# Kernel optimization log

Measured on AMD Instinct MI355X. Metric: run time of the kernel, lower is better.

Reference implementation:

```python
import jax, jax.numpy as jnp
import numpy as np

N_HEAD = 12
TOP_M = 16
MIN_SIZE = 2
MAX_SIZE = 8
ALPHA = 1.0
EPS = 1e-6

# Note: in the torch source, minimize_det=True and minimize_det=False select the
# identical subset (the sign flip in the score is exactly undone by flipping the
# comparisons), so we implement the single equivalent rule: maximize
# s = -log(det(K_S K_S^T) + 1e-6) / |S|**alpha.

def _token(qi, i, k_all, v_all):
    """Greedy DPP subset selection for one query token i. qi:[d], k_all/v_all:[T,d]."""
    T, d = k_all.shape
    slots = jnp.arange(MAX_SIZE)
    sim = k_all @ qi
    sim = jnp.where(jnp.arange(T) <= i, sim, -jnp.inf)  # causal mask
    vals, topidx = jax.lax.top_k(sim, TOP_M)
    avail0 = jnp.isfinite(vals) & (topidx != i)  # i is removed from candidates
    k_cand = k_all[topidx]                        # [M,d]
    cand_norm = jnp.sum(k_cand * k_cand, axis=-1)  # [M]
    ki = k_all[i]
    sel0 = jnp.zeros((MAX_SIZE,), jnp.int32).at[0].set(i.astype(jnp.int32))
    s0 = jax.lax.stop_gradient(-jnp.log(jnp.dot(ki, ki) + EPS))  # |S|=1 => size^alpha=1

    def body(state, _):
        sel, count, cur_s, avail, done = state
        # E: selected key vectors in slots < count, zeros elsewhere
        E = jnp.where((slots < count)[:, None], k_all[sel], 0.0)  # [S,d]
        G0 = E @ E.T                                              # [S,S]
        cross = k_cand @ E.T  # [M,S]; column `count` is 0 since that E row is 0
        u = (slots == count).astype(E.dtype)  # one-hot insertion slot
        # Gram of S u {c} for every candidate c, identity-padded beyond slot count
        grams = (G0[None]
                 + u[None, :, None] * cross[:, None, :]
                 + cross[:, :, None] * u[None, None, :]
                 + cand_norm[:, None, None] * (u[:, None] * u[None, :])[None])
        grams = grams + jnp.diag(jnp.where(slots > count, 1.0, 0.0))[None]
        det = jnp.linalg.det(grams.astype(jnp.float32))  # [M]
        s = -jnp.log(det + EPS) / (count + 1).astype(jnp.float32) ** ALPHA
        s = jax.lax.stop_gradient(jnp.where(avail, s, -jnp.inf))
        best = jnp.argmax(s)
        best_s = s[best]
        accept = (~done) & jnp.any(avail) & ((best_s > cur_s) | (count < MIN_SIZE))
        sel = jnp.where(accept & (slots == count), topidx[best].astype(jnp.int32), sel)
        avail = avail & ~(accept & (jnp.arange(TOP_M) == best))
        cur_s = jnp.where(accept, best_s, cur_s)
        count = count + accept.astype(count.dtype)
        done = done | ~accept
        return (sel, count, cur_s, avail, done), None

    init = (sel0, jnp.int32(1), s0, avail0, jnp.bool_(False))
    (sel, count, _, _, _), _ = jax.lax.scan(body, init, None, length=MAX_SIZE - 1)
    w = (slots < count).astype(v_all.dtype)
    return (v_all[sel] * w[:, None]).sum(0) / count.astype(v_all.dtype)

_tokens = jax.vmap(_token, in_axes=(0, 0, None, None))  # over T

def _head(qh, kh, vh):
    return _tokens(qh, jnp.arange(qh.shape[0]), kh, vh)

_attn = jax.vmap(jax.vmap(_head))  # over B, H

def _forward(x, W_attn, b_attn, W_proj, b_proj):
    B, T, C = x.shape
    hs = C // N_HEAD
    qkv = x @ W_attn + b_attn
    q, k, v = jnp.split(qkv, 3, axis=-1)
    q = q.reshape(B, T, N_HEAD, hs).transpose(0, 2, 1, 3)
    k = k.reshape(B, T, N_HEAD, hs).transpose(0, 2, 1, 3)
    v = v.reshape(B, T, N_HEAD, hs).transpose(0, 2, 1, 3)
    y = _attn(q, k, v)  # [B,H,T,hs]
    y = y.transpose(0, 2, 1, 3).reshape(B, T, C)
    return y @ W_proj + b_proj  # dropout=0.0 (eval)

def setup_inputs():
    key = jax.random.key(0)
    ks = jax.random.split(key, 3)
    B, T, C = 4, 512, 768
    return {
        "x": jax.random.normal(ks[0], (B, T, C), jnp.float32),
        "W_attn": jax.random.normal(ks[1], (C, 3 * C), jnp.float32) * 0.02,
        "b_attn": jnp.zeros((3 * C,), jnp.float32),
        "W_proj": jax.random.normal(ks[2], (C, C), jnp.float32) * 0.02,
        "b_proj": jnp.zeros((C,), jnp.float32),
    }

def reference(x, W_attn, b_attn, W_proj, b_proj):
    return _forward(x, W_attn, b_attn, W_proj, b_proj)
```

## Files before the change

kernel.cpp:

```cpp
#include <hip/hip_runtime.h>
#include <math.h>

constexpr int Bc = 4, Tc = 512, Cc = 768, Hc = 12, HSc = 64;
constexpr int QKVN = 3 * Cc;
constexpr double EPSd = 1e-6;

typedef unsigned short u16;
typedef __attribute__((ext_vector_type(8))) short short8;
typedef __attribute__((ext_vector_type(4))) float f32x4;

__device__ __forceinline__ u16 f2bf(float x) {
  unsigned u = __float_as_uint(x);
  return (u16)((u + 0x7FFFu + ((u >> 16) & 1u)) >> 16);
}
__device__ __forceinline__ float bf2f(u16 h) {
  return __uint_as_float((unsigned)h << 16);
}

__device__ __forceinline__ void gload16(const u16* g, u16* l) {
  __builtin_amdgcn_global_load_lds(
      (const __attribute__((address_space(1))) void*)g,
      (__attribute__((address_space(3))) void*)l, 16, 0, 0);
}

__global__ void __launch_bounds__(256) convsplit3(
    const float* __restrict__ in, u16* __restrict__ H, u16* __restrict__ M,
    u16* __restrict__ L) {
  const int i = blockIdx.x * 256 + threadIdx.x;
  const float4 v = ((const float4*)in)[i];
  const float x[4] = {v.x, v.y, v.z, v.w};
  ushort4 hv, mv, lv;
  u16* hp = (u16*)&hv; u16* mp = (u16*)&mv; u16* lp = (u16*)&lv;
#pragma unroll
  for (int c = 0; c < 4; ++c) {
    const u16 h = f2bf(x[c]);
    const float r1 = x[c] - bf2f(h);
    const u16 m = f2bf(r1);
    const u16 l = f2bf(r1 - bf2f(m));
    hp[c] = h; mp[c] = m; lp[c] = l;
  }
  ((ushort4*)H)[i] = hv;
  ((ushort4*)M)[i] = mv;
  ((ushort4*)L)[i] = lv;
}

__global__ void __launch_bounds__(256) convsplit3_t(
    const float* __restrict__ W, u16* __restrict__ Th, u16* __restrict__ Tm,
    u16* __restrict__ Tl, int K, int Nn) {
  __shared__ float t[64][65];
  const int k0 = blockIdx.x * 64, n0 = blockIdx.y * 64;
#pragma unroll
  for (int u = 0; u < 16; ++u) {
    const int idx = u * 256 + threadIdx.x;
    const int r = idx >> 6, c = idx & 63;
    t[r][c] = W[(size_t)(k0 + r) * Nn + n0 + c];
  }
  __syncthreads();
#pragma unroll
  for (int u = 0; u < 16; ++u) {
    const int idx = u * 256 + threadIdx.x;
    const int n = idx >> 6, k = idx & 63;
    const float x = t[k][n];
    const u16 h = f2bf(x);
    const float r1 = x - bf2f(h);
    const u16 m = f2bf(r1);
    const u16 l = f2bf(r1 - bf2f(m));
    Th[(size_t)(n0 + n) * K + k0 + k] = h;
    Tm[(size_t)(n0 + n) * K + k0 + k] = m;
    Tl[(size_t)(n0 + n) * K + k0 + k] = l;
  }
}

template <bool WRITE_PARTIAL>
__global__ void __launch_bounds__(128, 2) gemm_mfma3(
    const u16* __restrict__ A, const u16* __restrict__ B,
    const float* __restrict__ bias, float* __restrict__ outp,
    int N, int kPerSplit, int strideA, int strideB) {
  __shared__ __align__(16) u16 AsF[3 * 64 * 32];
  __shared__ __align__(16) u16 BsF[3 * 64 * 32];
  const int tid = threadIdx.x;
  const int wid = tid >> 6;
  const int lane = tid & 63;
  const int lm = lane & 15, kg = lane >> 4;
  const int rb = blockIdx.x * 64;
  const int cb = blockIdx.y * 64;
  const int kBeg = blockIdx.z * kPerSplit;

  const int trow = tid >> 2;
  const int tc4 = tid & 3;
  const int krot = ((tc4 - (trow >> 1)) & 3) * 8;
  const int sLds = tid * 8;
  int aOff = (rb + trow) * 768 + kBeg + krot;
  int bOff = (cb + trow) * 768 + kBeg + krot;

  f32x4 acc[2][4];
#pragma unroll
  for (int mf = 0; mf < 2; ++mf)
#pragma unroll
    for (int nf = 0; nf < 4; ++nf) acc[mf][nf] = (f32x4){0.f, 0.f, 0.f, 0.f};

  const int nIter = kPerSplit / 32;
  const int ckA = ((kg + (lm >> 1)) & 3) * 8;

  for (int it = 0; it < nIter; ++it) {
    __syncthreads();
#pragma unroll
    for (int u = 0; u < 6; ++u) {
      gload16(A + (size_t)(u >> 1) * strideA + (u & 1) * (32 * 768) + aOff,
              &AsF[(u >> 1) * 2048 + (u & 1) * 1024 + sLds]);
      gload16(B + (size_t)(u >> 1) * strideB + (u & 1) * (32 * 768) + bOff,
              &BsF[(u >> 1) * 2048 + (u & 1) * 1024 + sLds]);
    }
    aOff += 32; bOff += 32;
    __syncthreads();
    short8 ah[2], am[2], al[2];
#pragma unroll
    for (int mf = 0; mf < 2; ++mf) {
      const int ro = (wid * 32 + mf * 16 + lm) * 32 + ckA;
      ah[mf] = *(const short8*)&AsF[ro];
      am[mf] = *(const short8*)&AsF[2048 + ro];
      al[mf] = *(const short8*)&AsF[4096 + ro];
    }
#pragma unroll
    for (int nf = 0; nf < 4; ++nf) {
      const int co = (nf * 16 + lm) * 32 + ckA;
      const short8 bh = *(const short8*)&BsF[co];
      const short8 bm = *(const short8*)&BsF[2048 + co];
      const short8 bl = *(const short8*)&BsF[4096 + co];
#pragma unroll
      for (int mf = 0; mf < 2; ++mf) {
        acc[mf][nf] = __builtin_amdgcn_mfma_f32_16x16x32_bf16(
            al[mf], bh, acc[mf][nf], 0, 0, 0);
        acc[mf][nf] = __builtin_amdgcn_mfma_f32_16x16x32_bf16(
            ah[mf], bl, acc[mf][nf], 0, 0, 0);
        acc[mf][nf] = __builtin_amdgcn_mfma_f32_16x16x32_bf16(
            am[mf], bm, acc[mf][nf], 0, 0, 0);
        acc[mf][nf] = __builtin_amdgcn_mfma_f32_16x16x32_bf16(
            am[mf], bh, acc[mf][nf], 0, 0, 0);
        acc[mf][nf] = __builtin_amdgcn_mfma_f32_16x16x32_bf16(
            ah[mf], bm, acc[mf][nf], 0, 0, 0);
        acc[mf][nf] = __builtin_amdgcn_mfma_f32_16x16x32_bf16(
            ah[mf], bh, acc[mf][nf], 0, 0, 0);
      }
    }
  }

  const int colb = cb + lm;
  if (WRITE_PARTIAL) {
    float* Pp = outp + (size_t)blockIdx.z * 2048 * N;
#pragma unroll
    for (int mf = 0; mf < 2; ++mf)
#pragma unroll
      for (int r2 = 0; r2 < 4; ++r2) {
        float* orow =
            Pp + (size_t)(rb + wid * 32 + mf * 16 + kg * 4 + r2) * N + colb;
        orow[0]  = acc[mf][0][r2];
        orow[16] = acc[mf][1][r2];
        orow[32] = acc[mf][2][r2];
        orow[48] = acc[mf][3][r2];
      }
  } else {
    const float bb0 = bias[colb], bb1 = bias[colb + 16];
    const float bb2 = bias[colb + 32], bb3 = bias[colb + 48];
#pragma unroll
    for (int mf = 0; mf < 2; ++mf)
#pragma unroll
      for (int r2 = 0; r2 < 4; ++r2) {
        float* orow =
            outp + (size_t)(rb + wid * 32 + mf * 16 + kg * 4 + r2) * N + colb;
        orow[0]  = acc[mf][0][r2] + bb0;
        orow[16] = acc[mf][1][r2] + bb1;
        orow[32] = acc[mf][2][r2] + bb2;
        orow[48] = acc[mf][3][r2] + bb3;
      }
  }
}

__global__ void __launch_bounds__(256) reduce_bias_kernel(
    const float* __restrict__ P, const float* __restrict__ bias,
    float* __restrict__ outp, int MN, int N, int KS) {
  const int idx4 = (blockIdx.x * 256 + threadIdx.x) * 4;
  float4 acc = *(const float4*)&P[idx4];
  for (int ks = 1; ks < KS; ++ks) {
    const float4 p = *(const float4*)&P[(size_t)ks * MN + idx4];
    acc.x += p.x; acc.y += p.y; acc.z += p.z; acc.w += p.w;
  }
  const int col = idx4 % N;
  const float4 b4 = *(const float4*)&bias[col];
  acc.x += b4.x; acc.y += b4.y; acc.z += b4.z; acc.w += b4.w;
  *(float4*)&outp[idx4] = acc;
}

__global__ void __launch_bounds__(256) sims_kernel(
    const float* __restrict__ qkv, float* __restrict__ S) {
  const int bh = blockIdx.y;
  const int b = bh / Hc, h = bh % Hc;
  int it = 0;
  {
    const int t = blockIdx.x;
    while ((it + 1) * (it + 2) / 2 <= t) ++it;
  }
  const int jt = blockIdx.x - it * (it + 1) / 2;
  const int tid = threadIdx.x;
  const int tx = tid & 15, ty = tid >> 4;
  __shared__ float Qs[HSc][68];
  __shared__ float Ks[HSc][68];
  const float* base = qkv + (size_t)b * Tc * QKVN + h * HSc;
  {
    const int row = tid >> 2;
    const int d0 = (tid & 3) * 16;
    const float* qrow = base + (size_t)(it * 64 + row) * QKVN;
    const float* krow = base + (size_t)(jt * 64 + row) * QKVN + Cc;
#pragma unroll
    for (int u = 0; u < 4; ++u) {
      const float4 q4 = *(const float4*)&qrow[d0 + u * 4];
      const float4 k4 = *(const float4*)&krow[d0 + u * 4];
      Qs[d0 + u * 4 + 0][row] = q4.x; Qs[d0 + u * 4 + 1][row] = q4.y;
      Qs[d0 + u * 4 + 2][row] = q4.z; Qs[d0 + u * 4 + 3][row] = q4.w;
      Ks[d0 + u * 4 + 0][row] = k4.x; Ks[d0 + u * 4 + 1][row] = k4.y;
      Ks[d0 + u * 4 + 2][row] = k4.z; Ks[d0 + u * 4 + 3][row] = k4.w;
    }
  }
  __syncthreads();
  float acc[4][4];
#pragma unroll
  for (int m = 0; m < 4; ++m)
#pragma unroll
    for (int n = 0; n < 4; ++n) acc[m][n] = 0.0f;
#pragma unroll 4
  for (int d = 0; d < HSc; ++d) {
    const float4 a4 = *(const float4*)&Qs[d][ty * 4];
    const float4 b4 = *(const float4*)&Ks[d][tx * 4];
    const float a[4] = {a4.x, a4.y, a4.z, a4.w};
    const float bv[4] = {b4.x, b4.y, b4.z, b4.w};
#pragma unroll
    for (int m = 0; m < 4; ++m)
#pragma unroll
      for (int n = 0; n < 4; ++n) acc[m][n] += a[m] * bv[n];
  }
  float* Shead = S + (size_t)bh * Tc * Tc;
#pragma unroll
  for (int m = 0; m < 4; ++m) {
    const int i = it * 64 + ty * 4 + m;
    float4 o4 = {acc[m][0], acc[m][1], acc[m][2], acc[m][3]};
    *(float4*)&Shead[(size_t)i * Tc + jt * 64 + tx * 4] = o4;
  }
}

__global__ void __launch_bounds__(256) topk_kernel(
    const float* __restrict__ S, int* __restrict__ topidx,
    unsigned* __restrict__ availB) {
  const int tid = threadIdx.x;
  const int wv = tid >> 6, lane = tid & 63;
  const int tok = blockIdx.x * 4 + wv;
  const int i = tok & (Tc - 1);
  const float4* Sq = reinterpret_cast<const float4*>(S + (size_t)tok * Tc);
  unsigned long long key[8];
#pragma unroll
  for (int r = 0; r < 2; ++r) {
    const float4 v4 = Sq[lane * 2 + r];
    const float vv[4] = {v4.x, v4.y, v4.z, v4.w};
#pragma unroll
    for (int c = 0; c < 4; ++c) {
      const int j = lane * 8 + r * 4 + c;
      const unsigned u = __float_as_uint(vv[c]);
      const unsigned s = (u & 0x80000000u) ? ~u : (u | 0x80000000u);
      key[r * 4 + c] = (j <= i)
          ? (((unsigned long long)s << 32) | (unsigned)(511 - j))
          : 0ull;
    }
  }
  unsigned avail = 0;
  for (int m = 0; m < 16; ++m) {
    unsigned long long bk = 0;
#pragma unroll
    for (int r = 0; r < 8; ++r) bk = (key[r] > bk) ? key[r] : bk;
#pragma unroll
    for (int msk = 1; msk <= 32; msk <<= 1) {
      const unsigned long long ok = __shfl_xor(bk, msk);
      bk = (ok > bk) ? ok : bk;
    }
    const int j = 511 - (int)(unsigned)(bk & 0xFFFFFFFFull);
    const unsigned shi = (unsigned)(bk >> 32);
    if (lane == 0) topidx[(size_t)tok * 16 + m] = j & 511;
    if (shi > 0x007FFFFFu && j != i) avail |= (1u << m);
#pragma unroll
    for (int r = 0; r < 8; ++r) key[r] = (key[r] == bk) ? 0ull : key[r];
  }
  if (lane == 0) availB[tok] = avail;
}

__global__ void __launch_bounds__(256, 4) select_kernel(
    const float* __restrict__ qkv, const int* __restrict__ topidx,
    const unsigned* __restrict__ availB, u16* __restrict__ yh,
    u16* __restrict__ ym, u16* __restrict__ yl) {
  const int tid = threadIdx.x;
  const int wv = tid >> 6, lane = tid & 63;
  const int half = lane >> 5;
  const int l32 = lane & 31;
  const int m = l32 >> 1;
  const int q = l32 & 1;
  const int hbase = half << 5;

  const int tok = blockIdx.x * 8 + wv * 2 + half;
  const int bh = tok >> 9;
  const int i = tok & (Tc - 1);
  const int b = bh / Hc;
  const int h = bh % Hc;

  const float* base = qkv + (size_t)b * Tc * QKVN + h * HSc;
  const float* kbase = base + Cc;
  const float* vbase = base + 2 * Cc;

  const int tidx = topidx[(size_t)tok * 16 + m];
  unsigned avail = availB[tok];

  float kreg[32], kireg[32];
  {
    const float* kc = kbase + (size_t)tidx * QKVN + q * 32;
    const float* ki = kbase + (size_t)i * QKVN + q * 32;
#pragma unroll
    for (int u = 0; u < 8; ++u) {
      const float4 c4 = *(const float4*)&kc[u * 4];
      const float4 i4 = *(const float4*)&ki[u * 4];
      kreg[u * 4 + 0] = c4.x; kreg[u * 4 + 1] = c4.y;
      kreg[u * 4 + 2] = c4.z; kreg[u * 4 + 3] = c4.w;
      kireg[u * 4 + 0] = i4.x; kireg[u * 4 + 1] = i4.y;
      kireg[u * 4 + 2] = i4.z; kireg[u * 4 + 3] = i4.w;
    }
  }
  float cnorm_f = 0.0f, c0_f = 0.0f, kii_f = 0.0f;
#pragma unroll
  for (int e = 0; e < 32; ++e) {
    cnorm_f += kreg[e] * kreg[e];
    c0_f += kreg[e] * kireg[e];
    kii_f += kireg[e] * kireg[e];
  }
  cnorm_f += __shfl_xor(cnorm_f, 1);
  c0_f += __shfl_xor(c0_f, 1);
  kii_f += __shfl_xor(kii_f, 1);

  const double kii = (double)kii_f;
  double z[8];
#pragma unroll
  for (int t = 0; t < 8; ++t) z[t] = 0.0;
  z[0] = (double)c0_f / sqrt(kii);
  double schur = (double)cnorm_f - z[0] * z[0];
  double detS = kii;
  double Dprev = 0.0;
  int count = 1;
  int sel[8];
  sel[0] = i;
#pragma unroll
  for (int a = 1; a < 8; ++a) sel[a] = 0;
  bool hdone = false;

#pragma unroll
  for (int it = 0; it < 7; ++it) {
    const double D = detS * schur + EPSd;
    const bool act = ((avail >> m) & 1u) != 0;
    const bool bad = !(D > 0.0);
    double dkey = act ? (bad ? -INFINITY : D) : INFINITY;
    int bm = m;
#pragma unroll
    for (int msk = 2; msk <= 16; msk <<= 1) {
      const double ok2 = __shfl_xor(dkey, msk);
      const int om = __shfl_xor(bm, msk);
      const bool t2 = (ok2 < dkey) || (ok2 == dkey && om < bm);
      dkey = t2 ? ok2 : dkey;
      bm = t2 ? om : bm;
    }
    const double Dbest = __shfl(D, hbase | (bm * 2));
    bool acc_ok;
    if (it == 0) {
      acc_ok = true;
    } else {
      double pA = Dbest, pB = Dprev;
#pragma unroll
      for (int j = 0; j < it; ++j) pA *= Dbest;
#pragma unroll
      for (int j = 0; j < it + 1; ++j) pB *= Dprev;
      acc_ok = ((avail >> bm) & 1u) && (Dbest >= 0.0) && (Dprev >= 0.0) &&
               (pA < pB);
    }
    const bool X = !hdone && (avail != 0u) && acc_ok;
    hdone = hdone || !X;
    if (X) {
      float cp_f = 0.0f;
#pragma unroll
      for (int e = 0; e < 32; ++e) {
        const float kb = __shfl(kreg[e], hbase | (bm * 2) | q);
        cp_f += kreg[e] * kb;
      }
      cp_f += __shfl_xor(cp_f, 1);
      const double schur_b = __shfl(schur, hbase | (bm * 2));
      double sum = 0.0;
#pragma unroll
      for (int t = 0; t <= it; ++t) {
        const double zbt = __shfl(z[t], hbase | (bm * 2));
        sum += z[t] * zbt;
      }
      const double znew = ((double)cp_f - sum) / sqrt(schur_b);
      z[it + 1] = znew;
      schur -= znew * znew;
      detS *= schur_b;
      Dprev = Dbest;
      avail &= ~(1u << bm);
      ++count;
      sel[it + 1] = __shfl(tidx, hbase | (bm * 2));
    }
    if (__all(hdone)) break;
  }

  double acc0 = 0.0, acc1 = 0.0;
#pragma unroll
  for (int a = 0; a < 8; ++a)
    if (a < count) {
      const float* vrow = vbase + (size_t)sel[a] * QKVN;
      acc0 += (double)vrow[l32];
      acc1 += (double)vrow[l32 + 32];
    }
  const float v0 = (float)(acc0 / (double)count);
  const float v1 = (float)(acc1 / (double)count);
  const size_t yidx = (((size_t)b * Tc + i) * Hc + h) * HSc + l32;
  {
    const u16 hv = f2bf(v0);
    const float r1 = v0 - bf2f(hv);
    const u16 mv = f2bf(r1);
    yh[yidx] = hv; ym[yidx] = mv; yl[yidx] = f2bf(r1 - bf2f(mv));
  }
  {
    const u16 hv = f2bf(v1);
    const float r1 = v1 - bf2f(hv);
    const u16 mv = f2bf(r1);
    yh[yidx + 32] = hv; ym[yidx + 32] = mv;
    yl[yidx + 32] = f2bf(r1 - bf2f(mv));
  }
}

extern "C" void kernel_launch(void* const* d_in, const int* in_sizes, int n_in,
                              void* d_out, int out_size, void* d_ws, size_t ws_size,
                              hipStream_t stream) {
  (void)in_sizes; (void)n_in; (void)out_size; (void)ws_size;
  const float* x  = (const float*)d_in[0];
  const float* Wa = (const float*)d_in[1];
  const float* ba = (const float*)d_in[2];
  const float* Wp = (const float*)d_in[3];
  const float* bp = (const float*)d_in[4];
  float* out = (float*)d_out;

  constexpr size_t XPLANE = (size_t)Bc * Tc * Cc;
  constexpr size_t WAPLANE = (size_t)QKVN * Cc;
  constexpr size_t WPPLANE = (size_t)Cc * Cc;

  float* qkv = (float*)d_ws;
  int* topidx = (int*)(qkv + (size_t)Bc * Tc * QKVN);
  unsigned* availB = (unsigned*)(topidx + (size_t)Bc * Hc * Tc * 16);
  float* regionB = (float*)(availB + (size_t)Bc * Hc * Tc);
  float* S = regionB;
  float* Pproj = regionB;
  u16* Xh = (u16*)regionB;
  u16* Wath = Xh + 3 * XPLANE;
  u16* Wpth = (u16*)(regionB + (size_t)3 * 2048 * Cc);
  u16* yhp = Wpth + 3 * WPPLANE;

  const int MNproj = Bc * Tc * Cc;

  hipLaunchKernelGGL(convsplit3, dim3(1536), dim3(256), 0, stream,
                     x, Xh, Xh + XPLANE, Xh + 2 * XPLANE);
  hipLaunchKernelGGL(convsplit3_t, dim3(12, 36), dim3(256), 0, stream,
                     Wa, Wath, Wath + WAPLANE, Wath + 2 * WAPLANE, Cc, QKVN);
  hipLaunchKernelGGL((gemm_mfma3<false>), dim3(32, QKVN / 64, 1), dim3(128),
                     0, stream, Xh, Wath, ba, qkv, QKVN, Cc,
                     (int)XPLANE, (int)WAPLANE);
  hipLaunchKernelGGL(sims_kernel, dim3(36, Bc * Hc), dim3(256), 0,
                     stream, qkv, S);
  hipLaunchKernelGGL(topk_kernel, dim3(Bc * Hc * Tc / 4), dim3(256), 0,
                     stream, S, topidx, availB);
  hipLaunchKernelGGL(select_kernel, dim3(Bc * Hc * Tc / 8), dim3(256), 0,
                     stream, qkv, topidx, availB,
                     yhp, yhp + XPLANE, yhp + 2 * XPLANE);
  hipLaunchKernelGGL(convsplit3_t, dim3(12, 12), dim3(256), 0, stream,
                     Wp, Wpth, Wpth + WPPLANE, Wpth + 2 * WPPLANE, Cc, Cc);
  hipLaunchKernelGGL((gemm_mfma3<true>), dim3(32, Cc / 64, 3), dim3(128), 0,
                     stream, yhp, Wpth, nullptr, Pproj, Cc, 256,
                     (int)XPLANE, (int)WPPLANE);
  hipLaunchKernelGGL(reduce_bias_kernel, dim3(MNproj / 1024), dim3(256), 0,
                     stream, Pproj, bp, out, MNproj, Cc, 3);
}
```

Before: 281.0 us.

## Double-buffer LDS tiles in split-bf16 MFMA GEMM with vmcnt-based waits

The GEMM kernel's shared-memory tiles become two buffers. Global-to-LDS loads for the next K-step are issued before the current step is computed, and explicit s_waitcnt vmcnt counts wait only for the older batch. This is meant to overlap global memory latency with MFMA work instead of fully synchronizing around each load. It doubles LDS use per block, which may cut occupancy, and it assumes nIter is even and that vmcnt ordering holds for LDS-direct loads.

```diff
diff --git a/kernel.cpp b/kernel.cpp
--- a/kernel.cpp
+++ b/kernel.cpp
@@ -22,6 +22,9 @@
       (const __attribute__((address_space(1))) void*)g,
       (__attribute__((address_space(3))) void*)l, 16, 0, 0);
 }
+
+#define WAITVM12 asm volatile("s_waitcnt vmcnt(12)" ::: "memory")
+#define WAITVM0 asm volatile("s_waitcnt vmcnt(0)" ::: "memory")
 
 __global__ void __launch_bounds__(256) convsplit3(
     const float* __restrict__ in, u16* __restrict__ H, u16* __restrict__ M,
@@ -76,8 +79,8 @@
     const u16* __restrict__ A, const u16* __restrict__ B,
     const float* __restrict__ bias, float* __restrict__ outp,
     int N, int kPerSplit, int strideA, int strideB) {
-  __shared__ __align__(16) u16 AsF[3 * 64 * 32];
-  __shared__ __align__(16) u16 BsF[3 * 64 * 32];
+  __shared__ __align__(16) u16 AsF[2][3 * 64 * 32];
+  __shared__ __align__(16) u16 BsF[2][3 * 64 * 32];
   const int tid = threadIdx.x;
   const int wid = tid >> 6;
   const int lane = tid & 63;
@@ -102,31 +105,31 @@
   const int nIter = kPerSplit / 32;
   const int ckA = ((kg + (lm >> 1)) & 3) * 8;
 
-  for (int it = 0; it < nIter; ++it) {
-    __syncthreads();
+  auto stage = [&](int buf) {
 #pragma unroll
     for (int u = 0; u < 6; ++u) {
       gload16(A + (size_t)(u >> 1) * strideA + (u & 1) * (32 * 768) + aOff,
-              &AsF[(u >> 1) * 2048 + (u & 1) * 1024 + sLds]);
+              &AsF[buf][(u >> 1) * 2048 + (u & 1) * 1024 + sLds]);
       gload16(B + (size_t)(u >> 1) * strideB + (u & 1) * (32 * 768) + bOff,
-              &BsF[(u >> 1) * 2048 + (u & 1) * 1024 + sLds]);
+              &BsF[buf][(u >> 1) * 2048 + (u & 1) * 1024 + sLds]);
     }
     aOff += 32; bOff += 32;
-    __syncthreads();
+  };
+  auto compute = [&](int buf) {
     short8 ah[2], am[2], al[2];
 #pragma unroll
     for (int mf = 0; mf < 2; ++mf) {
       const int ro = (wid * 32 + mf * 16 + lm) * 32 + ckA;
-      ah[mf] = *(const short8*)&AsF[ro];
-      am[mf] = *(const short8*)&AsF[2048 + ro];
-      al[mf] = *(const short8*)&AsF[4096 + ro];
+      ah[mf] = *(const short8*)&AsF[buf][ro];
+      am[mf] = *(const short8*)&AsF[buf][2048 + ro];
+      al[mf] = *(const short8*)&AsF[buf][4096 + ro];
     }
 #pragma unroll
     for (int nf = 0; nf < 4; ++nf) {
       const int co = (nf * 16 + lm) * 32 + ckA;
-      const short8 bh = *(const short8*)&BsF[co];
-      const short8 bm = *(const short8*)&BsF[2048 + co];
-      const short8 bl = *(const short8*)&BsF[4096 + co];
+      const short8 bh = *(const short8*)&BsF[buf][co];
+      const short8 bm = *(const short8*)&BsF[buf][2048 + co];
+      const short8 bl = *(const short8*)&BsF[buf][4096 + co];
 #pragma unroll
       for (int mf = 0; mf < 2; ++mf) {
         acc[mf][nf] = __builtin_amdgcn_mfma_f32_16x16x32_bf16(
@@ -143,6 +146,21 @@
             ah[mf], bh, acc[mf][nf], 0, 0, 0);
       }
     }
+  };
+
+  stage(0);
+  stage(1);
+  for (int t = 0; t < nIter; t += 2) {
+    if (t + 1 < nIter) { WAITVM12; } else { WAITVM0; }
+    __builtin_amdgcn_s_barrier();
+    compute(0);
+    __builtin_amdgcn_s_barrier();
+    if (t + 2 < nIter) stage(0);
+    if (t + 2 < nIter) { WAITVM12; } else { WAITVM0; }
+    __builtin_amdgcn_s_barrier();
+    compute(1);
+    __builtin_amdgcn_s_barrier();
+    if (t + 3 < nIter) stage(1);
   }
 
   const int colb = cb + lm;
```

After: 299.1 us. 6.4% more time.
